# Kernel optimization log

Hardware: AMD Instinct MI355X
Metric: run time of the kernel (lower is better)

## Reference

```python
import jax, jax.numpy as jnp
import numpy as np

N, E, T, H, O, L = 8192, 262144, 256, 2048, 1024, 128


def setup_inputs() -> dict:
    key = jax.random.key(0)
    ks = jax.random.split(key, 24)
    inp = {}
    inp["eeg_nodes"] = jax.random.normal(ks[0], (N, T), dtype=jnp.float32)
    inp["eeg_idx"] = jax.random.randint(ks[1], (2, E), 0, N, dtype=jnp.int32)
    # PyG models.GIN layer widths: [T->2048], [2048->2048], [2048->2048], [2048->1024]
    dims = [(T, H), (H, H), (H, H), (H, O)]
    k = 2
    for l, (din, dh) in enumerate(dims):
        inp[f"w1_{l}"] = jax.random.normal(ks[k], (din, dh), jnp.float32) / np.float32(np.sqrt(din)); k += 1
        inp[f"b1_{l}"] = jnp.zeros((dh,), jnp.float32)
        inp[f"w2_{l}"] = jax.random.normal(ks[k], (dh, dh), jnp.float32) / np.float32(np.sqrt(dh)); k += 1
        inp[f"b2_{l}"] = jnp.zeros((dh,), jnp.float32)
    inp["wm"] = jax.random.normal(ks[k], (O, L), jnp.float32) / np.float32(np.sqrt(O)); k += 1
    inp["bm"] = jnp.zeros((L,), jnp.float32)
    inp["wv"] = jax.random.normal(ks[k], (O, L), jnp.float32) / np.float32(np.sqrt(O)); k += 1
    inp["bv"] = jnp.zeros((L,), jnp.float32)
    # reparameterize noise (torch.randn_like) made explicit for determinism
    inp["eps"] = jax.random.normal(ks[k + 1], (N, L), jnp.float32)
    return inp


def _gin_conv(x, src, dst, w1, b1, w2, b2):
    # GINConv, eps=0: mlp((1+0)*x + sum_{j->i} x_j); MLP = Linear-ReLU-Linear (no norm)
    agg = jax.ops.segment_sum(x[src], dst, num_segments=x.shape[0])  # [N, d]
    h = jax.nn.relu((x + agg) @ w1 + b1)
    return h @ w2 + b2


def reference(eeg_nodes, eeg_idx, w1_0, b1_0, w2_0, b2_0, w1_1, b1_1, w2_1, b2_1,
              w1_2, b1_2, w2_2, b2_2, w1_3, b1_3, w2_3, b2_3, wm, bm, wv, bv, eps):
    src, dst = eeg_idx[0], eeg_idx[1]
    layers = [(w1_0, b1_0, w2_0, b2_0), (w1_1, b1_1, w2_1, b2_1),
              (w1_2, b1_2, w2_2, b2_2), (w1_3, b1_3, w2_3, b2_3)]
    x = eeg_nodes
    for i, (w1, b1, w2, b2) in enumerate(layers):
        x = _gin_conv(x, src, dst, w1, b1, w2, b2)
        if i < len(layers) - 1:  # BasicGNN: ReLU between convs, not after last
            x = jax.nn.relu(x)
    mean = x @ wm + bm
    var = x @ wv + bv
    z = mean + var * eps  # reparameterize
    return (z, mean, var)
```

## Files before the change

kernel.cpp:

```cpp
#include <hip/hip_runtime.h>

#define NN 8192
#define EE 262144
#define TT 256
#define HH 2048
#define OO 1024
#define LL 128
#define NW 10

typedef __bf16 bf16_t;
typedef __bf16 bf16x8_t __attribute__((ext_vector_type(8)));
typedef float f32x4_t __attribute__((ext_vector_type(4)));

__device__ __forceinline__ void async16(void* lds, const void* g) {
  __builtin_amdgcn_global_load_lds(
      (const __attribute__((address_space(1))) void*)g,
      (__attribute__((address_space(3))) void*)lds, 16, 0, 0);
}


__global__ __launch_bounds__(256) void count_deg_kernel(const int* __restrict__ dst,
                                                        int* __restrict__ deg) {
  int e = blockIdx.x * 256 + threadIdx.x;
  if (e < EE) atomicAdd(&deg[dst[e]], 1);
}

__global__ __launch_bounds__(1024) void scan_kernel(const int* __restrict__ deg,
                                                    int* __restrict__ rs) {
  __shared__ int s[1024];
  int t = threadIdx.x;
  int pre[8];
  int sum = 0;
#pragma unroll
  for (int j = 0; j < 8; ++j) { pre[j] = sum; sum += deg[t * 8 + j]; }
  s[t] = sum;
  __syncthreads();
  for (int off = 1; off < 1024; off <<= 1) {
    int add = (t >= off) ? s[t - off] : 0;
    __syncthreads();
    s[t] += add;
    __syncthreads();
  }
  int base = (t == 0) ? 0 : s[t - 1];
#pragma unroll
  for (int j = 0; j < 8; ++j) rs[t * 8 + j] = base + pre[j];
  if (t == 1023) rs[8192] = s[1023];
}

__global__ __launch_bounds__(256) void fill_csr_kernel(const int* __restrict__ src,
                                                       const int* __restrict__ dst,
                                                       const int* __restrict__ rs,
                                                       int* __restrict__ cur,
                                                       int* __restrict__ csr) {
  int e = blockIdx.x * 256 + threadIdx.x;
  if (e >= EE) return;
  int d = dst[e];
  int p = atomicAdd(&cur[d], 1);
  csr[rs[d] + p] = src[e];
}

struct WTab {
  const float* src[NW];
  int K[NW];
  int N[NW];
  long long dstOff[NW];
  int tileStart[NW + 1];
  const float* x0;
  bf16_t* castDst;
  int castStart;
};

__global__ __launch_bounds__(256) void prep_all_kernel(WTab tab, bf16_t* __restrict__ WT) {
  int b = blockIdx.x;
  int t = threadIdx.x;
  if (b >= tab.castStart) {
    int i = (b - tab.castStart) * 256 + t;
    f32x4_t a = ((const f32x4_t*)tab.x0)[i * 2];
    f32x4_t bb = ((const f32x4_t*)tab.x0)[i * 2 + 1];
    bf16x8_t o;
#pragma unroll
    for (int j = 0; j < 4; ++j) { o[j] = (bf16_t)a[j]; o[4 + j] = (bf16_t)bb[j]; }
    ((bf16x8_t*)tab.castDst)[i] = o;
    return;
  }
  int wi = 0;
#pragma unroll
  for (int k = 1; k < NW; ++k)
    if (b >= tab.tileStart[k]) wi = k;
  int tt = b - tab.tileStart[wi];
  int K = tab.K[wi], N = tab.N[wi];
  int ntn = N >> 6;
  int n0 = (tt % ntn) * 64, k0 = (tt / ntn) * 64;
  const float* in = tab.src[wi];
  bf16_t* out = WT + tab.dstOff[wi];

  __shared__ float tile[64][65];
  for (int c = t; c < 1024; c += 256) {
    int r = c >> 4, col = (c & 15) * 4;
    f32x4_t v = *(const f32x4_t*)&in[(size_t)(k0 + r) * N + n0 + col];
#pragma unroll
    for (int j = 0; j < 4; ++j) tile[r][col + j] = v[j];
  }
  __syncthreads();
  for (int c = t; c < 512; c += 256) {
    int r = c >> 3, col = (c & 7) * 8;
    bf16x8_t v;
#pragma unroll
    for (int j = 0; j < 8; ++j) v[j] = (bf16_t)tile[col + j][r];
    *(bf16x8_t*)&out[(size_t)(n0 + r) * K + k0 + col] = v;
  }
}

__global__ __launch_bounds__(256) void transpose_cast_kernel(const float* __restrict__ in,
                                                             bf16_t* __restrict__ out,
                                                             int K, int N) {
  __shared__ float tile[64][65];
  int n0 = blockIdx.x * 64, k0 = blockIdx.y * 64;
  int t = threadIdx.x;
  for (int c = t; c < 1024; c += 256) {
    int r = c >> 4, col = (c & 15) * 4;
    f32x4_t v = *(const f32x4_t*)&in[(size_t)(k0 + r) * N + n0 + col];
#pragma unroll
    for (int j = 0; j < 4; ++j) tile[r][col + j] = v[j];
  }
  __syncthreads();
  for (int c = t; c < 512; c += 256) {
    int r = c >> 3, col = (c & 7) * 8;
    bf16x8_t v;
#pragma unroll
    for (int j = 0; j < 8; ++j) v[j] = (bf16_t)tile[col + j][r];
    *(bf16x8_t*)&out[(size_t)(n0 + r) * K + k0 + col] = v;
  }
}

__global__ __launch_bounds__(256) void cast_kernel(const float* __restrict__ in,
                                                   bf16_t* __restrict__ out) {
  int i = blockIdx.x * 256 + threadIdx.x;
  f32x4_t a = ((const f32x4_t*)in)[i * 2];
  f32x4_t b = ((const f32x4_t*)in)[i * 2 + 1];
  bf16x8_t o;
#pragma unroll
  for (int j = 0; j < 4; ++j) { o[j] = (bf16_t)a[j]; o[4 + j] = (bf16_t)b[j]; }
  ((bf16x8_t*)out)[i] = o;
}

__global__ __launch_bounds__(64) void agg0_kernel(const bf16_t* __restrict__ x,
                                                  bf16_t* __restrict__ out,
                                                  const int* __restrict__ rs,
                                                  const int* __restrict__ csr) {
  int t = threadIdx.x;
  int node = blockIdx.x * 2 + (t >> 5);
  int c = t & 31;
  const bf16x8_t* xv = (const bf16x8_t*)x;
  bf16x8_t self = xv[(size_t)node * 32 + c];
  float acc[8];
#pragma unroll
  for (int j = 0; j < 8; ++j) acc[j] = (float)self[j];
  int e0 = rs[node], e1 = rs[node + 1];
  int e = e0;
  for (; e + 4 <= e1; e += 4) {
    int s0 = csr[e], s1 = csr[e + 1], s2 = csr[e + 2], s3 = csr[e + 3];
    bf16x8_t v0 = xv[(size_t)s0 * 32 + c];
    bf16x8_t v1 = xv[(size_t)s1 * 32 + c];
    bf16x8_t v2 = xv[(size_t)s2 * 32 + c];
    bf16x8_t v3 = xv[(size_t)s3 * 32 + c];
#pragma unroll
    for (int j = 0; j < 8; ++j)
      acc[j] += (float)v0[j] + (float)v1[j] + (float)v2[j] + (float)v3[j];
  }
  for (; e < e1; ++e) {
    bf16x8_t v = xv[(size_t)csr[e] * 32 + c];
#pragma unroll
    for (int j = 0; j < 8; ++j) acc[j] += (float)v[j];
  }
  bf16x8_t o;
#pragma unroll
  for (int j = 0; j < 8; ++j) o[j] = (bf16_t)acc[j];
  ((bf16x8_t*)out)[(size_t)node * 32 + c] = o;
}

__global__ __launch_bounds__(256) void agg_tiled_kernel(const bf16_t* __restrict__ x,
                                                        bf16_t* __restrict__ out,
                                                        const int* __restrict__ rs,
                                                        const int* __restrict__ csr,
                                                        const float* __restrict__ bias,
                                                        int relu, int tmask, int tshift) {
  int t = threadIdx.x;
  int tile = blockIdx.x & tmask;
  int ng = blockIdx.x >> tshift;
  int node = ng * 8 + (t >> 5);
  int c = t & 31;
  size_t tb = (size_t)tile * (NN * 32);
  const bf16x8_t* xv = (const bf16x8_t*)x + tb;
  bf16x8_t self = xv[node * 32 + c];
  float acc[8];
#pragma unroll
  for (int j = 0; j < 8; ++j) acc[j] = (float)self[j];
  int e0 = rs[node], e1 = rs[node + 1];
  int e = e0;
  for (; e + 4 <= e1; e += 4) {
    int s0 = csr[e], s1 = csr[e + 1], s2 = csr[e + 2], s3 = csr[e + 3];
    bf16x8_t v0 = xv[s0 * 32 + c];
    bf16x8_t v1 = xv[s1 * 32 + c];
    bf16x8_t v2 = xv[s2 * 32 + c];
    bf16x8_t v3 = xv[s3 * 32 + c];
#pragma unroll
    for (int j = 0; j < 8; ++j)
      acc[j] += (float)v0[j] + (float)v1[j] + (float)v2[j] + (float)v3[j];
  }
  for (; e < e1; ++e) {
    bf16x8_t v = xv[csr[e] * 32 + c];
#pragma unroll
    for (int j = 0; j < 8; ++j) acc[j] += (float)v[j];
  }
  if (bias) {
    const float* bp = bias + tile * 256 + c * 8;
    f32x4_t b0 = *(const f32x4_t*)bp;
    f32x4_t b1 = *(const f32x4_t*)(bp + 4);
#pragma unroll
    for (int j = 0; j < 4; ++j) { acc[j] += b0[j]; acc[4 + j] += b1[j]; }
  }
  if (relu) {
#pragma unroll
    for (int j = 0; j < 8; ++j) acc[j] = fmaxf(acc[j], 0.f);
  }
  bf16x8_t o;
#pragma unroll
  for (int j = 0; j < 8; ++j) o[j] = (bf16_t)acc[j];
  ((bf16x8_t*)out + tb)[node * 32 + c] = o;
}

template <int CMODE>
__global__ __launch_bounds__(256, 2) void gemm_bt_kernel(
    const bf16_t* __restrict__ A, const bf16_t* __restrict__ Bt,
    const float* __restrict__ bias, const float* __restrict__ biasB,
    void* __restrict__ Cv, int N, int K, int relu, int nbxShift) {
  __shared__ __align__(16) bf16_t lA[128 * 32];
  __shared__ __align__(16) bf16_t lB[128 * 32];
  const int tid = threadIdx.x;
  const int lane = tid & 63;
  const int wave = tid >> 6;
  const int wm64 = (wave & 1) * 64;
  const int wn64 = (wave >> 1) * 64;
  const int row16 = lane & 15;
  const int quad = lane >> 4;

  const int bid = blockIdx.x;
  const int xcd = bid & 7;
  const int rank = bid >> 3;
  const int bn = rank & ((1 << nbxShift) - 1);
  const int mPer = gridDim.x >> (3 + nbxShift);
  const int bm = xcd * mPer + (rank >> nbxShift);
  const size_t m0 = (size_t)bm * 128;
  const size_t n0 = (size_t)bn * 128;

  f32x4_t acc[4][4];
#pragma unroll
  for (int i = 0; i < 4; ++i)
#pragma unroll
    for (int j = 0; j < 4; ++j)
#pragma unroll
      for (int r = 0; r < 4; ++r) acc[i][j][r] = 0.f;

  const bf16_t* Bbase = Bt + n0 * K;
  const int r0 = tid >> 2;
  const int r1 = (tid + 256) >> 2;
  const int kc = (tid & 3) * 8;

  for (int kt = 0; kt < K; kt += 32) {
    const bf16_t* Ab = A + ((size_t)(kt >> 8)) * (NN * 256) + (kt & 255) + kc;
    async16(&lA[tid * 8], Ab + (m0 + r0) * 256);
    async16(&lA[(tid + 256) * 8], Ab + (m0 + r1) * 256);
    async16(&lB[tid * 8], Bbase + (size_t)r0 * K + kt + kc);
    async16(&lB[(tid + 256) * 8], Bbase + (size_t)r1 * K + kt + kc);
    __syncthreads();
    bf16x8_t af[4], bfr[4];
#pragma unroll
    for (int i = 0; i < 4; ++i)
      af[i] = *(const bf16x8_t*)&lA[(wm64 + i * 16 + row16) * 32 + quad * 8];
#pragma unroll
    for (int i = 0; i < 4; ++i)
      bfr[i] = *(const bf16x8_t*)&lB[(wn64 + i * 16 + row16) * 32 + quad * 8];
#pragma unroll
    for (int i = 0; i < 4; ++i)
#pragma unroll
      for (int j = 0; j < 4; ++j)
        acc[i][j] = __builtin_amdgcn_mfma_f32_16x16x32_bf16(af[i], bfr[j], acc[i][j], 0, 0, 0);
    __syncthreads();
  }

#pragma unroll
  for (int i = 0; i < 4; ++i) {
    size_t row = m0 + wm64 + i * 16 + quad * 4;
#pragma unroll
    for (int j = 0; j < 4; ++j) {
      int col = (int)n0 + wn64 + j * 16 + row16;
      if (CMODE == 0) {
        float b = bias ? bias[col] : 0.f;
        size_t cb = ((size_t)(col >> 8)) * (NN * 256) + (col & 255);
#pragma unroll
        for (int r = 0; r < 4; ++r) {
          float o = acc[i][j][r] + b;
          if (relu) o = fmaxf(o, 0.f);
          ((bf16_t*)Cv)[cb + (row + r) * 256] = (bf16_t)o;
        }
      } else {
        int sel = col >> 7;
        int c2 = col & 127;
        float b = sel ? biasB[c2] : bias[c2];
        float* dstp = (float*)Cv + (size_t)(1 + sel) * NN * LL + c2;
#pragma unroll
        for (int r = 0; r < 4; ++r) {
          dstp[(row + r) * LL] = acc[i][j][r] + b;
        }
      }
    }
  }
}

__global__ __launch_bounds__(512, 2) void gemm256_kernel(
    const bf16_t* __restrict__ A, const bf16_t* __restrict__ Bt,
    const float* __restrict__ bias, bf16_t* __restrict__ C,
    int N, int K, int relu, int nbxShift) {
  __shared__ __align__(16) bf16_t lA[2][256 * 64];
  __shared__ __align__(16) bf16_t lB[2][256 * 64];

  const int t = threadIdx.x;
  const int lane = t & 63;
  const int wave = t >> 6;
  const int wm = wave >> 2;
  const int wn = wave & 3;
  const int row16 = lane & 15;
  const int quad = lane >> 4;
  const int sx = (row16 & 7) << 3;

  const int r0 = t >> 3;
  const int cs = ((t & 7) * 8) ^ ((r0 & 7) << 3);

  const int bid = blockIdx.x;
  const int xcd = bid & 7;
  const int rank = bid >> 3;
  const int bn = rank & ((1 << nbxShift) - 1);
  const int mPer = gridDim.x >> (3 + nbxShift);
  const int bm = xcd * mPer + (rank >> nbxShift);
  const size_t m0 = (size_t)bm * 256;
  const size_t n0 = (size_t)bn * 256;
  const int NT = K >> 6;

  f32x4_t acc[4][4][2];
#pragma unroll
  for (int Q = 0; Q < 4; ++Q)
#pragma unroll
    for (int i = 0; i < 4; ++i)
#pragma unroll
      for (int j = 0; j < 2; ++j)
#pragma unroll
        for (int r = 0; r < 4; ++r) acc[Q][i][j][r] = 0.f;

  bf16x8_t af[4][2], bf[2][2];

#define LOAD_A256(mh)                                                              \
  _Pragma("unroll") for (int i = 0; i < 4; ++i)                                    \
  _Pragma("unroll") for (int ks = 0; ks < 2; ++ks) {                               \
    int row_ = (mh)*128 + wm * 64 + i * 16 + row16;                                \
    af[i][ks] = *(const bf16x8_t*)&lA[c][row_ * 64 + ((ks * 32 + quad * 8) ^ sx)]; \
  }

#define LOAD_B256(nh)                                                              \
  _Pragma("unroll") for (int j = 0; j < 2; ++j)                                    \
  _Pragma("unroll") for (int ks = 0; ks < 2; ++ks) {                               \
    int row_ = (nh)*128 + wn * 32 + j * 16 + row16;                                \
    bf[j][ks] = *(const bf16x8_t*)&lB[c][row_ * 64 + ((ks * 32 + quad * 8) ^ sx)]; \
  }

#define STAGE_A256(U, mh)                                                            \
  {                                                                                  \
    int u_ = (U);                                                                    \
    int us_ = u_ < NT ? u_ : NT - 1;                                                 \
    int kt_ = us_ << 6;                                                              \
    const bf16_t* g_ = A + (size_t)(kt_ >> 8) * (NN * 256) + (m0 + (mh)*128) * 256 + \
                       (kt_ & 255) + cs;                                             \
    bf16_t* l_ = &lA[u_ & 1][(mh)*8192];                                             \
    async16(l_ + (size_t)t * 8, g_ + (size_t)r0 * 256);                              \
    async16(l_ + (size_t)(t + 512) * 8, g_ + (size_t)(r0 + 64) * 256);               \
  }

#define STAGE_B256(U, nh)                                                  \
  {                                                                        \
    int u_ = (U);                                                          \
    int us_ = u_ < NT ? u_ : NT - 1;                                       \
    int kt_ = us_ << 6;                                                    \
    const bf16_t* g_ = Bt + (n0 + (nh)*128) * (size_t)K + kt_ + cs;        \
    bf16_t* l_ = &lB[u_ & 1][(nh)*8192];                                   \
    async16(l_ + (size_t)t * 8, g_ + (size_t)r0 * K);                      \
    async16(l_ + (size_t)(t + 512) * 8, g_ + (size_t)(r0 + 64) * K);       \
  }

#define MFMA_Q(Q)                                                                    \
  __builtin_amdgcn_s_setprio(1);                                                     \
  _Pragma("unroll") for (int i = 0; i < 4; ++i)                                      \
  _Pragma("unroll") for (int j = 0; j < 2; ++j)                                      \
  _Pragma("unroll") for (int ks = 0; ks < 2; ++ks)                                   \
      acc[Q][i][j] =                                                                 \
          __builtin_amdgcn_mfma_f32_16x16x32_bf16(af[i][ks], bf[j][ks], acc[Q][i][j],\
                                                  0, 0, 0);                          \
  __builtin_amdgcn_s_setprio(0);

#define BAR asm volatile("s_barrier" ::: "memory")

  STAGE_A256(0, 0); STAGE_B256(0, 0); STAGE_A256(0, 1); STAGE_B256(0, 1);
  asm volatile("" ::: "memory");
  STAGE_A256(1, 0); STAGE_B256(1, 0);
  asm volatile("s_waitcnt vmcnt(4)" ::: "memory");
  BAR;

  for (int T = 0; T < NT; ++T) {
    const int c = T & 1;
    LOAD_A256(0); LOAD_B256(0);
    STAGE_A256(T + 1, 1); STAGE_B256(T + 1, 1);
    BAR;
    MFMA_Q(0);
    BAR;
    LOAD_B256(1);
    BAR;
    MFMA_Q(1);
    BAR;
    LOAD_A256(1); LOAD_B256(0);
    STAGE_A256(T + 2, 0);
    BAR;
    MFMA_Q(2);
    BAR;
    LOAD_B256(1);
    STAGE_B256(T + 2, 0);
    BAR;
    MFMA_Q(3);
    asm volatile("s_waitcnt vmcnt(4)" ::: "memory");
    BAR;
  }
  asm volatile("s_waitcnt vmcnt(0)" ::: "memory");

#pragma unroll
  for (int Q = 0; Q < 4; ++Q) {
    const int mh = Q >> 1, nh = Q & 1;
#pragma unroll
    for (int i = 0; i < 4; ++i) {
      size_t row = m0 + mh * 128 + wm * 64 + i * 16 + quad * 4;
#pragma unroll
      for (int j = 0; j < 2; ++j) {
        int col = (int)n0 + nh * 128 + wn * 32 + j * 16 + row16;
        float b = bias ? bias[col] : 0.f;
        size_t cb = ((size_t)(col >> 8)) * (NN * 256) + (col & 255);
#pragma unroll
        for (int r = 0; r < 4; ++r) {
          float o = acc[Q][i][j][r] + b;
          if (relu) o = fmaxf(o, 0.f);
          C[cb + (row + r) * 256] = (bf16_t)o;
        }
      }
    }
  }
#undef LOAD_A256
#undef LOAD_B256
#undef STAGE_A256
#undef STAGE_B256
#undef MFMA_Q
#undef BAR
}

__global__ __launch_bounds__(256) void reparam_kernel(const float* __restrict__ mean,
                                                      const float* __restrict__ var,
                                                      const float* __restrict__ eps,
                                                      float* __restrict__ z) {
  int i = blockIdx.x * 256 + threadIdx.x;
  f32x4_t m = ((const f32x4_t*)mean)[i];
  f32x4_t v = ((const f32x4_t*)var)[i];
  f32x4_t e = ((const f32x4_t*)eps)[i];
  f32x4_t o;
#pragma unroll
  for (int j = 0; j < 4; ++j) o[j] = m[j] + v[j] * e[j];
  ((f32x4_t*)z)[i] = o;
}

extern "C" void kernel_launch(void* const* d_in, const int* in_sizes, int n_in,
                              void* d_out, int out_size, void* d_ws, size_t ws_size,
                              hipStream_t stream) {
  (void)in_sizes; (void)n_in; (void)out_size;
  const float* x0 = (const float*)d_in[0];
  const int* ei = (const int*)d_in[1];
  const int* src = ei;
  const int* dst = ei + EE;
  const float* w1[4] = {(const float*)d_in[2], (const float*)d_in[6],
                        (const float*)d_in[10], (const float*)d_in[14]};
  const float* b1[4] = {(const float*)d_in[3], (const float*)d_in[7],
                        (const float*)d_in[11], (const float*)d_in[15]};
  const float* w2[4] = {(const float*)d_in[4], (const float*)d_in[8],
                        (const float*)d_in[12], (const float*)d_in[16]};
  const float* b2[4] = {(const float*)d_in[5], (const float*)d_in[9],
                        (const float*)d_in[13], (const float*)d_in[17]};
  const float* wm = (const float*)d_in[18];
  const float* bm = (const float*)d_in[19];
  const float* wv = (const float*)d_in[20];
  const float* bv = (const float*)d_in[21];
  const float* eps = (const float*)d_in[22];
  float* out = (float*)d_out;

  char* ws = (char*)d_ws;
  bf16_t* B0 = (bf16_t*)(ws);
  bf16_t* B1 = (bf16_t*)(ws + 33554432);
  bf16_t* WT = (bf16_t*)(ws + 67108864);

  const long long soff[NW] = {0LL, 524288LL, 4718592LL, 8912896LL, 13107200LL,
                              17301504LL, 21495808LL, 23592960LL, 24641536LL, 24772608LL};
  const size_t wtBytesFull = 24903680ULL * 2ULL;
  const size_t needFull = 67108864ULL + wtBytesFull + 2097152ULL;
  bool full = ws_size >= needFull;

  size_t csrBase = full ? (67108864ULL + wtBytesFull) : 75497472ULL;
  int* deg = (int*)(ws + csrBase);
  int* cur = deg + 8192;
  int* rs = deg + 16384;
  int* csr = deg + 16384 + 8200;

  auto AGG = [&](const bf16_t* in, bf16_t* outp, int d, const float* bias, int relu) {
    int ntiles = d >> 8;
    int tshift = (ntiles == 8) ? 3 : 2;
    agg_tiled_kernel<<<(NN / 8) * ntiles, 256, 0, stream>>>(in, outp, rs, csr, bias, relu,
                                                            ntiles - 1, tshift);
  };

  if (full) {
    WTab tab;
    const float* srcs[NW] = {w1[0], w2[0], w1[1], w2[1], w1[2], w2[2], w1[3], w2[3], wm, wv};
    const int Ks[NW] = {TT, HH, HH, HH, HH, HH, HH, OO, OO, OO};
    const int Ns[NW] = {HH, HH, HH, HH, HH, HH, OO, OO, LL, LL};
    int cum = 0;
    for (int i = 0; i < NW; ++i) {
      tab.src[i] = srcs[i];
      tab.K[i] = Ks[i];
      tab.N[i] = Ns[i];
      tab.dstOff[i] = soff[i];
      tab.tileStart[i] = cum;
      cum += (Ns[i] >> 6) * (Ks[i] >> 6);
    }
    tab.tileStart[NW] = cum;
    tab.castStart = cum;
    tab.x0 = x0;
    tab.castDst = B0;
    int totalBlocks = cum + (NN * TT / 8) / 256;
    prep_all_kernel<<<totalBlocks, 256, 0, stream>>>(tab, WT);

    hipMemsetAsync(deg, 0, 2 * 8192 * sizeof(int), stream);
    count_deg_kernel<<<EE / 256, 256, 0, stream>>>(dst, deg);
    scan_kernel<<<1, 1024, 0, stream>>>(deg, rs);
    fill_csr_kernel<<<EE / 256, 256, 0, stream>>>(src, dst, rs, cur, csr);

    auto G2 = [&](const bf16_t* Ain, int wi, const float* bias, bf16_t* Cout, int K, int relu) {
      gemm256_kernel<<<8 * (NN / 256), 512, 0, stream>>>(Ain, WT + soff[wi], bias, Cout,
                                                         HH, K, relu, 3);
    };
    auto G = [&](const bf16_t* Ain, int wi, const float* bias, bf16_t* Cout, int Nn, int K,
                 int relu) {
      int nbx = Nn / 128;
      int shift = __builtin_ctz(nbx);
      gemm_bt_kernel<0><<<nbx * (NN / 128), 256, 0, stream>>>(
          Ain, WT + soff[wi], bias, nullptr, (void*)Cout, Nn, K, relu, shift);
    };

    agg0_kernel<<<NN / 2, 64, 0, stream>>>(B0, B1, rs, csr);
    G2(B1, 0, b1[0], B0, TT, 1);
    G2(B0, 1, b2[0], B1, HH, 1);
    AGG(B1, B0, HH, nullptr, 0);
    G2(B0, 2, b1[1], B1, HH, 1);
    G2(B1, 3, b2[1], B0, HH, 1);
    AGG(B0, B1, HH, nullptr, 0);
    G2(B1, 4, b1[2], B0, HH, 1);
    G2(B0, 5, b2[2], B1, HH, 1);
    G(B1, 6, nullptr, B0, OO, HH, 0);
    AGG(B0, B1, OO, b1[3], 1);
    G(B1, 7, b2[3], B0, OO, OO, 0);
    gemm_bt_kernel<1><<<2 * (NN / 128), 256, 0, stream>>>(
        B0, WT + soff[8], bm, bv, (void*)out, 256, OO, 0, 1);
  } else {
    hipMemsetAsync(deg, 0, 2 * 8192 * sizeof(int), stream);
    count_deg_kernel<<<EE / 256, 256, 0, stream>>>(dst, deg);
    scan_kernel<<<1, 1024, 0, stream>>>(deg, rs);
    fill_csr_kernel<<<EE / 256, 256, 0, stream>>>(src, dst, rs, cur, csr);

    auto T = [&](const float* w, int K, int Nn, bf16_t* dstw) {
      transpose_cast_kernel<<<dim3(Nn / 64, K / 64), 256, 0, stream>>>(w, dstw, K, Nn);
    };
    auto G2 = [&](const bf16_t* Ain, const float* bias, bf16_t* Cout, int K, int relu) {
      gemm256_kernel<<<8 * (NN / 256), 512, 0, stream>>>(Ain, WT, bias, Cout, HH, K, relu, 3);
    };
    auto G = [&](const bf16_t* Ain, const float* bias, bf16_t* Cout, int Nn, int K, int relu) {
      int nbx = Nn / 128;
      int shift = __builtin_ctz(nbx);
      gemm_bt_kernel<0><<<nbx * (NN / 128), 256, 0, stream>>>(
          Ain, WT, bias, nullptr, (void*)Cout, Nn, K, relu, shift);
    };

    cast_kernel<<<(NN * TT / 8) / 256, 256, 0, stream>>>(x0, B0);
    agg0_kernel<<<NN / 2, 64, 0, stream>>>(B0, B1, rs, csr);
    T(w1[0], TT, HH, WT); G2(B1, b1[0], B0, TT, 1);
    T(w2[0], HH, HH, WT); G2(B0, b2[0], B1, HH, 1);
    AGG(B1, B0, HH, nullptr, 0);
    T(w1[1], HH, HH, WT); G2(B0, b1[1], B1, HH, 1);
    T(w2[1], HH, HH, WT); G2(B1, b2[1], B0, HH, 1);
    AGG(B0, B1, HH, nullptr, 0);
    T(w1[2], HH, HH, WT); G2(B1, b1[2], B0, HH, 1);
    T(w2[2], HH, HH, WT); G2(B0, b2[2], B1, HH, 1);
    T(w1[3], HH, OO, WT); G(B1, nullptr, B0, OO, HH, 0);
    AGG(B0, B1, OO, b1[3], 1);
    T(w2[3], OO, OO, WT); G(B1, b2[3], B0, OO, OO, 0);
    T(wm, OO, LL, WT);
    T(wv, OO, LL, WT + (size_t)LL * OO);
    gemm_bt_kernel<1><<<2 * (NN / 128), 256, 0, stream>>>(
        B0, WT, bm, bv, (void*)out, 256, OO, 0, 1);
  }

  reparam_kernel<<<(NN * LL / 4) / 256, 256, 0, stream>>>(
      out + (size_t)NN * LL, out + (size_t)2 * NN * LL, eps, out);
}
```

Baseline: 812.1 us.

## Restructure gemm256 main loop to cut barriers and keep both B halves in registers

```diff
diff --git a/kernel.cpp b/kernel.cpp
--- a/kernel.cpp
+++ b/kernel.cpp
@@ -318,7 +318,7 @@
   }
 }
 
-__global__ __launch_bounds__(512, 2) void gemm256_kernel(
+__global__ __launch_bounds__(512, 1) void gemm256_kernel(
     const bf16_t* __restrict__ A, const bf16_t* __restrict__ Bt,
     const float* __restrict__ bias, bf16_t* __restrict__ C,
     int N, int K, int relu, int nbxShift) {
@@ -357,7 +357,7 @@
 #pragma unroll
         for (int r = 0; r < 4; ++r) acc[Q][i][j][r] = 0.f;
 
-  bf16x8_t af[4][2], bf[2][2];
+  bf16x8_t af[4][2], bf[4][2];
 
 #define LOAD_A256(mh)                                                              \
   _Pragma("unroll") for (int i = 0; i < 4; ++i)                                    \
@@ -366,11 +366,12 @@
     af[i][ks] = *(const bf16x8_t*)&lA[c][row_ * 64 + ((ks * 32 + quad * 8) ^ sx)]; \
   }
 
-#define LOAD_B256(nh)                                                              \
+#define LOAD_B256H(nh)                                                             \
   _Pragma("unroll") for (int j = 0; j < 2; ++j)                                    \
   _Pragma("unroll") for (int ks = 0; ks < 2; ++ks) {                               \
     int row_ = (nh)*128 + wn * 32 + j * 16 + row16;                                \
-    bf[j][ks] = *(const bf16x8_t*)&lB[c][row_ * 64 + ((ks * 32 + quad * 8) ^ sx)]; \
+    bf[(nh)*2 + j][ks] =                                                           \
+        *(const bf16x8_t*)&lB[c][row_ * 64 + ((ks * 32 + quad * 8) ^ sx)];         \
   }
 
 #define STAGE_A256(U, mh)                                                            \
@@ -401,12 +402,16 @@
   _Pragma("unroll") for (int i = 0; i < 4; ++i)                                      \
   _Pragma("unroll") for (int j = 0; j < 2; ++j)                                      \
   _Pragma("unroll") for (int ks = 0; ks < 2; ++ks)                                   \
-      acc[Q][i][j] =                                                                 \
-          __builtin_amdgcn_mfma_f32_16x16x32_bf16(af[i][ks], bf[j][ks], acc[Q][i][j],\
-                                                  0, 0, 0);                          \
+      acc[Q][i][j] = __builtin_amdgcn_mfma_f32_16x16x32_bf16(                        \
+          af[i][ks], bf[(Q & 1) * 2 + j][ks], acc[Q][i][j], 0, 0, 0);                \
   __builtin_amdgcn_s_setprio(0);
 
-#define BAR asm volatile("s_barrier" ::: "memory")
+#define BAR                                                                \
+  do {                                                                     \
+    __builtin_amdgcn_sched_barrier(0);                                     \
+    asm volatile("s_barrier" ::: "memory");                                \
+    __builtin_amdgcn_sched_barrier(0);                                     \
+  } while (0)
 
   STAGE_A256(0, 0); STAGE_B256(0, 0); STAGE_A256(0, 1); STAGE_B256(0, 1);
   asm volatile("" ::: "memory");
@@ -416,24 +421,23 @@
 
   for (int T = 0; T < NT; ++T) {
     const int c = T & 1;
-    LOAD_A256(0); LOAD_B256(0);
-    STAGE_A256(T + 1, 1); STAGE_B256(T + 1, 1);
+    LOAD_A256(0);
+    LOAD_B256H(0);
+    STAGE_A256(T + 1, 1);
+    MFMA_Q(0);
+    __builtin_amdgcn_sched_barrier(0);
+    LOAD_B256H(1);
     BAR;
-    MFMA_Q(0);
+    STAGE_B256(T + 1, 1);
+    MFMA_Q(1);
+    __builtin_amdgcn_sched_barrier(0);
+    LOAD_A256(1);
     BAR;
-    LOAD_B256(1);
-    BAR;
-    MFMA_Q(1);
-    BAR;
-    LOAD_A256(1); LOAD_B256(0);
     STAGE_A256(T + 2, 0);
-    BAR;
     MFMA_Q(2);
-    BAR;
-    LOAD_B256(1);
     STAGE_B256(T + 2, 0);
-    BAR;
     MFMA_Q(3);
+    __builtin_amdgcn_sched_barrier(0);
     asm volatile("s_waitcnt vmcnt(4)" ::: "memory");
     BAR;
   }
@@ -460,7 +464,7 @@
     }
   }
 #undef LOAD_A256
-#undef LOAD_B256
+#undef LOAD_B256H
 #undef STAGE_A256
 #undef STAGE_B256
 #undef MFMA_Q
```

Result: no change. 809.9 us (-0.3%).
